# Optimization experiments

Hardware: AMD Instinct MI355X
Metric: run time of the kernel (lower is better)

The kernel has to match this reference:

```python
import jax, jax.numpy as jnp
import numpy as np

B, L, D, H = 2, 4096, 512, 8
HD = D // H  # head_dim = 64


def setup_inputs() -> dict:
    key = jax.random.key(0)
    ks = jax.random.split(key, 5)
    s = 0.02
    return {
        "x": jax.random.normal(ks[0], (B, L, D), dtype=jnp.float32),
        "w_qkv": jax.random.normal(ks[1], (D, 3 * D), dtype=jnp.float32) * s,
        "b_qkv": jax.random.normal(ks[2], (3 * D,), dtype=jnp.float32) * s,
        "w_o": jax.random.normal(ks[3], (D, D), dtype=jnp.float32) * s,
        "b_o": jax.random.normal(ks[4], (D,), dtype=jnp.float32) * s,
    }


def reference(x, w_qkv, b_qkv, w_o, b_o):
    b, l, _ = x.shape
    # QKV projection, then split heads: [B, L, 3D] -> [B, H, L, 3*HD]
    qkv = x @ w_qkv + b_qkv
    qkv = qkv.reshape(b, l, H, 3 * HD).transpose(0, 2, 1, 3)
    q, k, v = jnp.split(qkv, 3, axis=-1)  # each [B, H, L, HD]
    scale = 1.0 / jnp.sqrt(jnp.asarray(HD, dtype=q.dtype))
    # full score matrix [B, H, L, L], softmax in float32 (matches .float() cast)
    scores = jnp.einsum('bhld,bhsd->bhls', q, k) * scale
    attn = jax.nn.softmax(scores.astype(jnp.float32), axis=-1).astype(q.dtype)
    values = jnp.einsum('bhls,bhsd->bhld', attn, v)  # [B, H, L, HD]
    values = values.transpose(0, 2, 1, 3).reshape(b, l, D)
    return values @ w_o + b_o
```

## Files before the change

### kernel.cpp

```cpp
#include <hip/hip_runtime.h>


#define B_  2
#define L_  4096
#define D_  512
#define H_  8
#define HD_ 64
#define BH_ (B_*H_)
#define M_  (B_*L_)
#define QKVN (3*D_)
#define HEADSZ (BH_*L_*HD_)

typedef unsigned short ushort;
typedef unsigned int uint;
typedef __bf16 bf16x8 __attribute__((ext_vector_type(8)));
typedef float  f32x4  __attribute__((ext_vector_type(4)));
typedef float  f32x16 __attribute__((ext_vector_type(16)));

typedef const __attribute__((address_space(1))) void g_void;
typedef __attribute__((address_space(3))) void l_void;

#define C2_ 0.18033688011112042f

#if __has_builtin(__builtin_amdgcn_exp2f)
#define FEXP2(x) __builtin_amdgcn_exp2f(x)
#else
#define FEXP2(x) exp2f(x)
#endif

__device__ __forceinline__ ushort f2bf(float f) {
    __bf16 h = (__bf16)f;
    return __builtin_bit_cast(ushort, h);
}

__device__ __forceinline__ uint pack2(float lo, float hi) {
    return (uint)f2bf(lo) | ((uint)f2bf(hi) << 16);
}

__global__ __launch_bounds__(256)
void prep_k(const float* __restrict__ x, ushort* __restrict__ xb,
            const float* __restrict__ wq, ushort* __restrict__ wtq,
            const float* __restrict__ wo, ushort* __restrict__ wto)
{
    int bid = blockIdx.x, tid = threadIdx.x;
    if (bid < 4096) {
        int idx = bid * 256 + tid;
        float4 v = ((const float4*)x)[idx];
        ushort4 o; o.x = f2bf(v.x); o.y = f2bf(v.y); o.z = f2bf(v.z); o.w = f2bf(v.w);
        ((ushort4*)xb)[idx] = o;
    } else if (bid < 7168) {
        int idx = (bid - 4096) * 256 + tid;
        int c = idx / D_, r = idx % D_;
        wtq[idx] = f2bf(wq[r * QKVN + c]);
    } else {
        int idx = (bid - 7168) * 256 + tid;
        int c = idx / D_, r = idx % D_;
        wto[idx] = f2bf(wo[r * D_ + c]);
    }
}

template<int BN>
__global__ __launch_bounds__(256)
void gemm_bt(const ushort* __restrict__ A, const ushort* __restrict__ Bt,
             const float* __restrict__ bias, void* __restrict__ out,
             int M, int N, int K, int mode)
{
    constexpr int MT = (BN == 128) ? 4 : 2;
    constexpr int BL = BN / 64;
    __shared__ ushort As[2][128 * 32];
    __shared__ ushort Bs[2][BN * 32];

    const int tid  = threadIdx.x;
    const int lane = tid & 63;
    const int wid  = tid >> 6;
    const int wm   = (BN == 128) ? (wid >> 1) : wid;
    const int wn   = (BN == 128) ? (wid & 1) : 0;
    const int lr   = lane & 15;
    const int quad = lane >> 4;
    const int tm = blockIdx.x, tn = blockIdx.y;

    f32x4 acc[MT][4] = {};
    const int arow = tm * 128;
    const int brow = tn * BN;

    auto STAGE = [&](int t) {
        const int k0 = t * 32;
        ushort* as = &As[t & 1][0];
        ushort* bs = &Bs[t & 1][0];
        #pragma unroll
        for (int i = 0; i < 2; i++) {
            int c   = i * 256 + tid;
            int row = c >> 2;
            int kk  = (c & 3) * 8;
            __builtin_amdgcn_global_load_lds(
                (g_void*)&A[(size_t)(arow + row) * K + k0 + kk],
                (l_void*)&as[c * 8], 16, 0, 0);
        }
        #pragma unroll
        for (int i = 0; i < BL; i++) {
            int c   = i * 256 + tid;
            int row = c >> 2;
            int kk  = (c & 3) * 8;
            __builtin_amdgcn_global_load_lds(
                (g_void*)&Bt[(size_t)(brow + row) * K + k0 + kk],
                (l_void*)&bs[c * 8], 16, 0, 0);
        }
    };

    const int NK = K / 32;
    STAGE(0);
    for (int t = 0; t < NK; t++) {
        __syncthreads();
        if (t + 1 < NK) STAGE(t + 1);
        const ushort* as = &As[t & 1][0];
        const ushort* bs = &Bs[t & 1][0];

        bf16x8 af[MT], bfr[4];
        #pragma unroll
        for (int mt = 0; mt < MT; mt++)
            af[mt] = *(const bf16x8*)&as[(wm * (MT * 16) + mt * 16 + lr) * 32 + quad * 8];
        #pragma unroll
        for (int nt = 0; nt < 4; nt++)
            bfr[nt] = *(const bf16x8*)&bs[(wn * 64 + nt * 16 + lr) * 32 + quad * 8];
        #pragma unroll
        for (int mt = 0; mt < MT; mt++)
            #pragma unroll
            for (int nt = 0; nt < 4; nt++)
                acc[mt][nt] = __builtin_amdgcn_mfma_f32_16x16x32_bf16(
                    af[mt], bfr[nt], acc[mt][nt], 0, 0, 0);
    }

    if (mode == 0) {
        #pragma unroll
        for (int nt = 0; nt < 4; nt++) {
            int col = tn * BN + wn * 64 + nt * 16 + lr;
            float bv = bias[col];
            #pragma unroll
            for (int mt = 0; mt < MT; mt++) {
                #pragma unroll
                for (int r = 0; r < 4; r++) {
                    int row = tm * 128 + wm * (MT * 16) + mt * 16 + quad * 4 + r;
                    ((float*)out)[(size_t)row * N + col] = acc[mt][nt][r] + bv;
                }
            }
        }
    } else {
        const int g     = (tn * BN + wn * 64) >> 6;
        const int which = g % 3;
        const int h     = g / 3;
        ushort* qkv = (ushort*)out;
        if (which != 2) {
            const float qscale = (which == 0) ? C2_ : 1.0f;
            #pragma unroll
            for (int nt = 0; nt < 4; nt++) {
                int d = nt * 16 + lr;
                float bv = bias[g * 64 + d];
                #pragma unroll
                for (int mt = 0; mt < MT; mt++) {
                    #pragma unroll
                    for (int r = 0; r < 4; r++) {
                        int row = tm * 128 + wm * (MT * 16) + mt * 16 + quad * 4 + r;
                        int b = row >> 12;
                        int l = row & (L_ - 1);
                        float v = (acc[mt][nt][r] + bv) * qscale;
                        qkv[which * HEADSZ + (((b * H_ + h) * L_ + l) * HD_) + d]
                            = f2bf(v);
                    }
                }
            }
        } else {
            ushort* vt = qkv + 2 * HEADSZ;
            #pragma unroll
            for (int nt = 0; nt < 4; nt++) {
                int d = nt * 16 + lr;
                float bv = bias[g * 64 + d];
                #pragma unroll
                for (int mt = 0; mt < MT; mt++) {
                    int row0 = tm * 128 + wm * (MT * 16) + mt * 16 + quad * 4;
                    int b = row0 >> 12;
                    int l = row0 & (L_ - 1);
                    ushort4 pk;
                    pk.x = f2bf(acc[mt][nt][0] + bv);
                    pk.y = f2bf(acc[mt][nt][1] + bv);
                    pk.z = f2bf(acc[mt][nt][2] + bv);
                    pk.w = f2bf(acc[mt][nt][3] + bv);
                    *(ushort4*)&vt[((size_t)(b * H_ + h) * HD_ + d) * L_ + l] = pk;
                }
            }
        }
    }
}

__global__ __launch_bounds__(512, 4)
void attn_k(const ushort* __restrict__ Q, const ushort* __restrict__ K,
            const ushort* __restrict__ VT, ushort* __restrict__ O)
{
    __shared__ __align__(16) ushort SMEM[24576];
    ushort* Ksm = SMEM;
    ushort* Vsm = SMEM + 8192;

    const int tid  = threadIdx.x;
    const int lane = tid & 63;
    const int wid  = tid >> 6;
    const int qw   = wid & 3;
    const int kh   = wid >> 2;
    const int l31  = lane & 31;
    const int hi   = lane >> 5;

    const int wg  = blockIdx.x;
    const int xcd = wg & 7, sl = wg >> 3;
    const int bh  = (xcd << 1) | (sl >> 5);
    const int q0  = (sl & 31) * 128;
    const size_t base = (size_t)bh * (L_ * HD_);

    const int sr = tid >> 3;
    const int sc = ((tid & 7) ^ (sr & 7)) * 8;
    const ushort* Kg = K  + base + sr * HD_ + sc;
    const ushort* Vg = VT + base + (size_t)sr * L_ + sc;

    bf16x8 qf[4];
    {
        const ushort* qp = Q + base + (size_t)(q0 + qw * 32 + l31) * HD_ + hi * 8;
        #pragma unroll
        for (int ks = 0; ks < 4; ks++) qf[ks] = *(const bf16x8*)(qp + ks * 16);
    }

    const int swz = (l31 & 7) << 4;
    int cbe[4];
    #pragma unroll
    for (int ks = 0; ks < 4; ks++) cbe[ks] = ((ks * 32 + hi * 16) ^ swz) >> 1;
    const int krW  = (kh * 32 + l31) * 64;
    const int kr0v = l31 * 64, kr1v = (32 + l31) * 64;

    const f32x16 Z = {};
    bf16x8 onesB;
    #pragma unroll
    for (int i = 0; i < 8; i++) onesB[i] = (__bf16)1.0f;

    f32x16 o0 = {}, o1 = {}, l_acc = {};
    f32x16 sE, sO;

    auto STAGE = [&](int tt) {
        __builtin_amdgcn_global_load_lds(
            (g_void*)(Kg + (size_t)tt * 64 * HD_),
            (l_void*)(Ksm + (tt & 1) * 4096 + tid * 8), 16, 0, 0);
        __builtin_amdgcn_global_load_lds(
            (g_void*)(Vg + tt * 64),
            (l_void*)(Vsm + (tt & 3) * 4096 + tid * 8), 16, 0, 0);
    };

    auto QK = [&](int tt, f32x16& S) {
        const ushort* kb = Ksm + (tt & 1) * 4096;
        {
            bf16x8 k0 = *(const bf16x8*)&kb[krW + cbe[0]];
            S = __builtin_amdgcn_mfma_f32_32x32x16_bf16(k0, qf[0], Z, 0, 0, 0);
        }
        #pragma unroll
        for (int ks = 1; ks < 4; ks++) {
            bf16x8 k0 = *(const bf16x8*)&kb[krW + cbe[ks]];
            S = __builtin_amdgcn_mfma_f32_32x32x16_bf16(k0, qf[ks], S, 0, 0, 0);
        }
    };

    auto SMPV = [&](int tp, f32x16& S) {
        const ushort* vb = Vsm + (tp & 3) * 4096;
        #pragma unroll
        for (int i = 0; i < 16; i++) S[i] = FEXP2(S[i]);
        #pragma unroll
        for (int kk = 0; kk < 2; kk++) {
            const int ks = kh * 2 + kk;
            const int r0 = 8 * kk;
            uint a0 = pack2(S[r0 + 0], S[r0 + 1]);
            uint a1 = pack2(S[r0 + 2], S[r0 + 3]);
            uint b0 = pack2(S[r0 + 4], S[r0 + 5]);
            uint b1 = pack2(S[r0 + 6], S[r0 + 7]);
            asm("v_permlane32_swap_b32 %0, %1" : "+v"(a0), "+v"(b0));
            asm("v_permlane32_swap_b32 %0, %1" : "+v"(a1), "+v"(b1));
            uint4 w; w.x = a0; w.y = a1; w.z = b0; w.w = b1;
            bf16x8 pa = __builtin_bit_cast(bf16x8, w);
            bf16x8 v0 = *(const bf16x8*)&vb[kr0v + cbe[ks]];
            bf16x8 v1 = *(const bf16x8*)&vb[kr1v + cbe[ks]];
            o0 = __builtin_amdgcn_mfma_f32_32x32x16_bf16(pa, v0, o0, 0, 0, 0);
            o1 = __builtin_amdgcn_mfma_f32_32x32x16_bf16(pa, v1, o1, 0, 0, 0);
            l_acc = __builtin_amdgcn_mfma_f32_32x32x16_bf16(pa, onesB, l_acc, 0, 0, 0);
        }
    };

    STAGE(0);

    for (int t = 0; t < L_ / 64; t += 2) {
        __syncthreads();
        STAGE(t + 1);
        QK(t, sE);
        if (t > 0) SMPV(t - 1, sO);
        __syncthreads();
        if (t + 2 < L_ / 64) STAGE(t + 2);
        QK(t + 1, sO);
        SMPV(t, sE);
    }
    SMPV(L_ / 64 - 1, sO);

    __syncthreads();
    float* red = (float*)SMEM;
    if (kh == 1) {
        float* p = red + (qw * 64 + lane) * 48;
        #pragma unroll
        for (int r = 0; r < 16; r++) {
            p[r] = o0[r]; p[16 + r] = o1[r]; p[32 + r] = l_acc[r];
        }
    }
    __syncthreads();
    if (kh == 0) {
        const float* p = red + (qw * 64 + lane) * 48;
        #pragma unroll
        for (int r = 0; r < 16; r++) {
            o0[r] += p[r]; o1[r] += p[16 + r]; l_acc[r] += p[32 + r];
        }
        const int b = bh >> 3, h = bh & 7;
        #pragma unroll
        for (int r = 0; r < 16; r++) {
            const int qrl = (r & 3) + 8 * (r >> 2) + 4 * hi;
            const float inv = 1.0f / l_acc[r];
            const size_t row = (size_t)(b * L_ + q0 + qw * 32 + qrl) * D_ + h * HD_ + l31;
            O[row]      = f2bf(o0[r] * inv);
            O[row + 32] = f2bf(o1[r] * inv);
        }
    }
}

extern "C" void kernel_launch(void* const* d_in, const int* in_sizes, int n_in,
                              void* d_out, int out_size, void* d_ws, size_t ws_size,
                              hipStream_t stream)
{
    const float* x     = (const float*)d_in[0];
    const float* w_qkv = (const float*)d_in[1];
    const float* b_qkv = (const float*)d_in[2];
    const float* w_o   = (const float*)d_in[3];
    const float* b_o   = (const float*)d_in[4];

    char* ws = (char*)d_ws;
    size_t o = 0;
    ushort* xb   = (ushort*)(ws + o); o += (size_t)M_ * D_ * 2;
    ushort* qkv  = (ushort*)(ws + o); o += (size_t)3 * HEADSZ * 2;
    ushort* attn = (ushort*)(ws + o); o += (size_t)M_ * D_ * 2;
    ushort* wtq  = (ushort*)(ws + o); o += (size_t)QKVN * D_ * 2;
    ushort* wto  = (ushort*)(ws + o);

    hipLaunchKernelGGL(prep_k, dim3(8192), dim3(256), 0, stream,
                       x, xb, w_qkv, wtq, w_o, wto);
    hipLaunchKernelGGL((gemm_bt<128>), dim3(M_ / 128, QKVN / 128), dim3(256), 0, stream,
                       xb, wtq, b_qkv, (void*)qkv, M_, QKVN, D_, 1);
    hipLaunchKernelGGL(attn_k, dim3(512), dim3(512), 0, stream,
                       qkv, qkv + HEADSZ, qkv + 2 * HEADSZ, attn);
    hipLaunchKernelGGL((gemm_bt<64>), dim3(M_ / 128, D_ / 64), dim3(256), 0, stream,
                       attn, wto, b_o, d_out, M_, D_, D_, 0);
}
```

Measured before the change: 204.3 us.

## Fuse prep, QKV GEMM, attention and output GEMM into one persistent kernel

```diff
diff --git a/kernel.cpp b/kernel.cpp
--- a/kernel.cpp
+++ b/kernel.cpp
@@ -10,6 +10,7 @@
 #define M_  (B_*L_)
 #define QKVN (3*D_)
 #define HEADSZ (BH_*L_*HD_)
+#define NBLK 512
 
 typedef unsigned short ushort;
 typedef unsigned int uint;
@@ -37,148 +38,152 @@
     return (uint)f2bf(lo) | ((uint)f2bf(hi) << 16);
 }
 
-__global__ __launch_bounds__(256)
-void prep_k(const float* __restrict__ x, ushort* __restrict__ xb,
-            const float* __restrict__ wq, ushort* __restrict__ wtq,
-            const float* __restrict__ wo, ushort* __restrict__ wto)
+__device__ uint g_cnt[4] = {0, 0, 0, 0};
+__device__ uint g_gen[4] = {0, 0, 0, 0};
+
+__device__ __forceinline__ void gbar(int i) {
+    __syncthreads();
+    if (threadIdx.x == 0) {
+        uint gen = __hip_atomic_load(&g_gen[i], __ATOMIC_ACQUIRE,
+                                     __HIP_MEMORY_SCOPE_AGENT);
+        __threadfence();
+        uint old = __hip_atomic_fetch_add(&g_cnt[i], 1u, __ATOMIC_ACQ_REL,
+                                          __HIP_MEMORY_SCOPE_AGENT);
+        if (old == (uint)NBLK - 1u) {
+            __hip_atomic_store(&g_cnt[i], 0u, __ATOMIC_RELAXED,
+                               __HIP_MEMORY_SCOPE_AGENT);
+            __hip_atomic_store(&g_gen[i], gen + 1u, __ATOMIC_RELEASE,
+                               __HIP_MEMORY_SCOPE_AGENT);
+        } else {
+            for (long k = 0; k < 10000000L; ++k) {
+                if (__hip_atomic_load(&g_gen[i], __ATOMIC_ACQUIRE,
+                                      __HIP_MEMORY_SCOPE_AGENT) != gen) break;
+                __builtin_amdgcn_s_sleep(4);
+            }
+        }
+        __threadfence();
+    }
+    __syncthreads();
+}
+
+__global__ __launch_bounds__(512, 4)
+void fused_k(const float* __restrict__ x,  const float* __restrict__ wq,
+             const float* __restrict__ bq, const float* __restrict__ wo,
+             const float* __restrict__ bo, char* __restrict__ ws,
+             float* __restrict__ out)
 {
-    int bid = blockIdx.x, tid = threadIdx.x;
-    if (bid < 4096) {
-        int idx = bid * 256 + tid;
-        float4 v = ((const float4*)x)[idx];
-        ushort4 o; o.x = f2bf(v.x); o.y = f2bf(v.y); o.z = f2bf(v.z); o.w = f2bf(v.w);
-        ((ushort4*)xb)[idx] = o;
-    } else if (bid < 7168) {
-        int idx = (bid - 4096) * 256 + tid;
-        int c = idx / D_, r = idx % D_;
-        wtq[idx] = f2bf(wq[r * QKVN + c]);
-    } else {
-        int idx = (bid - 7168) * 256 + tid;
-        int c = idx / D_, r = idx % D_;
-        wto[idx] = f2bf(wo[r * D_ + c]);
-    }
-}
-
-template<int BN>
-__global__ __launch_bounds__(256)
-void gemm_bt(const ushort* __restrict__ A, const ushort* __restrict__ Bt,
-             const float* __restrict__ bias, void* __restrict__ out,
-             int M, int N, int K, int mode)
-{
-    constexpr int MT = (BN == 128) ? 4 : 2;
-    constexpr int BL = BN / 64;
-    __shared__ ushort As[2][128 * 32];
-    __shared__ ushort Bs[2][BN * 32];
+    __shared__ __align__(16) ushort SMEM[24576];
+
+    ushort* xb  = (ushort*)ws;
+    ushort* qkv = (ushort*)(ws + (size_t)M_ * D_ * 2);
+    ushort* aO  = qkv + (size_t)3 * HEADSZ;
+    ushort* wtq = aO + (size_t)M_ * D_;
+    ushort* wto = wtq + (size_t)QKVN * D_;
 
     const int tid  = threadIdx.x;
+    const int wg   = blockIdx.x;
     const int lane = tid & 63;
     const int wid  = tid >> 6;
-    const int wm   = (BN == 128) ? (wid >> 1) : wid;
-    const int wn   = (BN == 128) ? (wid & 1) : 0;
     const int lr   = lane & 15;
     const int quad = lane >> 4;
-    const int tm = blockIdx.x, tn = blockIdx.y;
-
-    f32x4 acc[MT][4] = {};
-    const int arow = tm * 128;
-    const int brow = tn * BN;
-
-    auto STAGE = [&](int t) {
-        const int k0 = t * 32;
-        ushort* as = &As[t & 1][0];
-        ushort* bs = &Bs[t & 1][0];
-        #pragma unroll
-        for (int i = 0; i < 2; i++) {
-            int c   = i * 256 + tid;
-            int row = c >> 2;
-            int kk  = (c & 3) * 8;
-            __builtin_amdgcn_global_load_lds(
-                (g_void*)&A[(size_t)(arow + row) * K + k0 + kk],
-                (l_void*)&as[c * 8], 16, 0, 0);
-        }
-        #pragma unroll
-        for (int i = 0; i < BL; i++) {
-            int c   = i * 256 + tid;
-            int row = c >> 2;
-            int kk  = (c & 3) * 8;
-            __builtin_amdgcn_global_load_lds(
-                (g_void*)&Bt[(size_t)(brow + row) * K + k0 + kk],
-                (l_void*)&bs[c * 8], 16, 0, 0);
-        }
-    };
-
-    const int NK = K / 32;
-    STAGE(0);
-    for (int t = 0; t < NK; t++) {
-        __syncthreads();
-        if (t + 1 < NK) STAGE(t + 1);
-        const ushort* as = &As[t & 1][0];
-        const ushort* bs = &Bs[t & 1][0];
-
-        bf16x8 af[MT], bfr[4];
-        #pragma unroll
-        for (int mt = 0; mt < MT; mt++)
-            af[mt] = *(const bf16x8*)&as[(wm * (MT * 16) + mt * 16 + lr) * 32 + quad * 8];
-        #pragma unroll
-        for (int nt = 0; nt < 4; nt++)
-            bfr[nt] = *(const bf16x8*)&bs[(wn * 64 + nt * 16 + lr) * 32 + quad * 8];
-        #pragma unroll
-        for (int mt = 0; mt < MT; mt++)
-            #pragma unroll
-            for (int nt = 0; nt < 4; nt++)
-                acc[mt][nt] = __builtin_amdgcn_mfma_f32_16x16x32_bf16(
-                    af[mt], bfr[nt], acc[mt][nt], 0, 0, 0);
+
+    {
+        const int gtid = wg * 512 + tid;
+        #pragma unroll
+        for (int i = 0; i < 4; i++) {
+            int idx = i * 262144 + gtid;
+            float4 v = ((const float4*)x)[idx];
+            ushort4 o4; o4.x = f2bf(v.x); o4.y = f2bf(v.y);
+            o4.z = f2bf(v.z); o4.w = f2bf(v.w);
+            ((ushort4*)xb)[idx] = o4;
+        }
+        #pragma unroll
+        for (int i = 0; i < 3; i++) {
+            int idx = i * 262144 + gtid;
+            int c = idx / D_, r = idx % D_;
+            wtq[idx] = f2bf(wq[r * QKVN + c]);
+        }
+        {
+            int c = gtid / D_, r = gtid % D_;
+            wto[gtid] = f2bf(wo[r * D_ + c]);
+        }
     }
-
-    if (mode == 0) {
-        #pragma unroll
-        for (int nt = 0; nt < 4; nt++) {
-            int col = tn * BN + wn * 64 + nt * 16 + lr;
-            float bv = bias[col];
-            #pragma unroll
-            for (int mt = 0; mt < MT; mt++) {
+    gbar(0);
+
+    {
+        ushort* As = SMEM;
+        ushort* Bs = SMEM + 16384;
+        const int wm = wid >> 1, wn = wid & 1;
+        const int tm = wg >> 4, tn = wg & 15;
+        const int arow = tm * 256, brow = tn * 96;
+        f32x4 acc[4][3] = {};
+
+        auto STAGE = [&](int t) {
+            const int k0 = t * 32;
+            ushort* as = As + (t & 1) * 8192;
+            ushort* bs = Bs + (t & 1) * 3072;
+            #pragma unroll
+            for (int i = 0; i < 2; i++) {
+                int c = i * 512 + tid, row = c >> 2, kk = (c & 3) * 8;
+                __builtin_amdgcn_global_load_lds(
+                    (g_void*)&xb[(size_t)(arow + row) * D_ + k0 + kk],
+                    (l_void*)&as[c * 8], 16, 0, 0);
+            }
+            if (tid < 384) {
+                int c = tid, row = c >> 2, kk = (c & 3) * 8;
+                __builtin_amdgcn_global_load_lds(
+                    (g_void*)&wtq[(size_t)(brow + row) * D_ + k0 + kk],
+                    (l_void*)&bs[c * 8], 16, 0, 0);
+            }
+        };
+
+        STAGE(0);
+        for (int t = 0; t < 16; t++) {
+            __syncthreads();
+            if (t + 1 < 16) STAGE(t + 1);
+            const ushort* as = As + (t & 1) * 8192;
+            const ushort* bs = Bs + (t & 1) * 3072;
+            bf16x8 af[4], bfr[3];
+            #pragma unroll
+            for (int mt = 0; mt < 4; mt++)
+                af[mt] = *(const bf16x8*)&as[(wm * 64 + mt * 16 + lr) * 32 + quad * 8];
+            #pragma unroll
+            for (int nt = 0; nt < 3; nt++)
+                bfr[nt] = *(const bf16x8*)&bs[(wn * 48 + nt * 16 + lr) * 32 + quad * 8];
+            #pragma unroll
+            for (int mt = 0; mt < 4; mt++)
                 #pragma unroll
-                for (int r = 0; r < 4; r++) {
-                    int row = tm * 128 + wm * (MT * 16) + mt * 16 + quad * 4 + r;
-                    ((float*)out)[(size_t)row * N + col] = acc[mt][nt][r] + bv;
-                }
-            }
-        }
-    } else {
-        const int g     = (tn * BN + wn * 64) >> 6;
-        const int which = g % 3;
-        const int h     = g / 3;
-        ushort* qkv = (ushort*)out;
-        if (which != 2) {
-            const float qscale = (which == 0) ? C2_ : 1.0f;
-            #pragma unroll
-            for (int nt = 0; nt < 4; nt++) {
-                int d = nt * 16 + lr;
-                float bv = bias[g * 64 + d];
+                for (int nt = 0; nt < 3; nt++)
+                    acc[mt][nt] = __builtin_amdgcn_mfma_f32_16x16x32_bf16(
+                        af[mt], bfr[nt], acc[mt][nt], 0, 0, 0);
+        }
+
+        #pragma unroll
+        for (int nt = 0; nt < 3; nt++) {
+            const int col0  = tn * 96 + wn * 48 + nt * 16;
+            const int g     = col0 >> 6;
+            const int which = g % 3;
+            const int h     = g / 3;
+            const int d     = (col0 & 63) + lr;
+            const float bv  = bq[col0 + lr];
+            if (which != 2) {
+                const float qs = (which == 0) ? C2_ : 1.0f;
                 #pragma unroll
-                for (int mt = 0; mt < MT; mt++) {
+                for (int mt = 0; mt < 4; mt++) {
                     #pragma unroll
                     for (int r = 0; r < 4; r++) {
-                        int row = tm * 128 + wm * (MT * 16) + mt * 16 + quad * 4 + r;
-                        int b = row >> 12;
-                        int l = row & (L_ - 1);
-                        float v = (acc[mt][nt][r] + bv) * qscale;
+                        int row = tm * 256 + wm * 64 + mt * 16 + quad * 4 + r;
+                        int b = row >> 12, l = row & (L_ - 1);
                         qkv[which * HEADSZ + (((b * H_ + h) * L_ + l) * HD_) + d]
-                            = f2bf(v);
+                            = f2bf((acc[mt][nt][r] + bv) * qs);
                     }
                 }
-            }
-        } else {
-            ushort* vt = qkv + 2 * HEADSZ;
-            #pragma unroll
-            for (int nt = 0; nt < 4; nt++) {
-                int d = nt * 16 + lr;
-                float bv = bias[g * 64 + d];
+            } else {
+                ushort* vt = qkv + 2 * HEADSZ;
                 #pragma unroll
-                for (int mt = 0; mt < MT; mt++) {
-                    int row0 = tm * 128 + wm * (MT * 16) + mt * 16 + quad * 4;
-                    int b = row0 >> 12;
-                    int l = row0 & (L_ - 1);
+                for (int mt = 0; mt < 4; mt++) {
+                    int row0 = tm * 256 + wm * 64 + mt * 16 + quad * 4;
+                    int b = row0 >> 12, l = row0 & (L_ - 1);
                     ushort4 pk;
                     pk.x = f2bf(acc[mt][nt][0] + bv);
                     pk.y = f2bf(acc[mt][nt][1] + bv);
@@ -189,141 +194,192 @@
             }
         }
     }
-}
-
-__global__ __launch_bounds__(512, 4)
-void attn_k(const ushort* __restrict__ Q, const ushort* __restrict__ K,
-            const ushort* __restrict__ VT, ushort* __restrict__ O)
-{
-    __shared__ __align__(16) ushort SMEM[24576];
-    ushort* Ksm = SMEM;
-    ushort* Vsm = SMEM + 8192;
-
-    const int tid  = threadIdx.x;
-    const int lane = tid & 63;
-    const int wid  = tid >> 6;
-    const int qw   = wid & 3;
-    const int kh   = wid >> 2;
-    const int l31  = lane & 31;
-    const int hi   = lane >> 5;
-
-    const int wg  = blockIdx.x;
-    const int xcd = wg & 7, sl = wg >> 3;
-    const int bh  = (xcd << 1) | (sl >> 5);
-    const int q0  = (sl & 31) * 128;
-    const size_t base = (size_t)bh * (L_ * HD_);
-
-    const int sr = tid >> 3;
-    const int sc = ((tid & 7) ^ (sr & 7)) * 8;
-    const ushort* Kg = K  + base + sr * HD_ + sc;
-    const ushort* Vg = VT + base + (size_t)sr * L_ + sc;
-
-    bf16x8 qf[4];
+    gbar(1);
+
     {
-        const ushort* qp = Q + base + (size_t)(q0 + qw * 32 + l31) * HD_ + hi * 8;
-        #pragma unroll
-        for (int ks = 0; ks < 4; ks++) qf[ks] = *(const bf16x8*)(qp + ks * 16);
+        ushort* Ksm = SMEM;
+        ushort* Vsm = SMEM + 8192;
+
+        const int qw  = wid & 3;
+        const int kh  = wid >> 2;
+        const int l31 = lane & 31;
+        const int hi  = lane >> 5;
+
+        const int xcd = wg & 7, sl = wg >> 3;
+        const int bh  = (xcd << 1) | (sl >> 5);
+        const int q0  = (sl & 31) * 128;
+        const size_t base = (size_t)bh * (L_ * HD_);
+
+        const int sr = tid >> 3;
+        const int sc = ((tid & 7) ^ (sr & 7)) * 8;
+        const ushort* Q  = qkv;
+        const ushort* K  = qkv + HEADSZ;
+        const ushort* VT = qkv + 2 * HEADSZ;
+        const ushort* Kg = K  + base + sr * HD_ + sc;
+        const ushort* Vg = VT + base + (size_t)sr * L_ + sc;
+
+        bf16x8 qf[4];
+        {
+            const ushort* qp = Q + base + (size_t)(q0 + qw * 32 + l31) * HD_ + hi * 8;
+            #pragma unroll
+            for (int ks = 0; ks < 4; ks++) qf[ks] = *(const bf16x8*)(qp + ks * 16);
+        }
+
+        const int swz = (l31 & 7) << 4;
+        int cbe[4];
+        #pragma unroll
+        for (int ks = 0; ks < 4; ks++) cbe[ks] = ((ks * 32 + hi * 16) ^ swz) >> 1;
+        const int krW  = (kh * 32 + l31) * 64;
+        const int kr0v = l31 * 64, kr1v = (32 + l31) * 64;
+
+        const f32x16 Z = {};
+        bf16x8 onesB;
+        #pragma unroll
+        for (int i = 0; i < 8; i++) onesB[i] = (__bf16)1.0f;
+
+        f32x16 o0 = {}, o1 = {}, l_acc = {};
+        f32x16 sE, sO;
+
+        auto STAGE = [&](int tt) {
+            __builtin_amdgcn_global_load_lds(
+                (g_void*)(Kg + (size_t)tt * 64 * HD_),
+                (l_void*)(Ksm + (tt & 1) * 4096 + tid * 8), 16, 0, 0);
+            __builtin_amdgcn_global_load_lds(
+                (g_void*)(Vg + tt * 64),
+                (l_void*)(Vsm + (tt & 3) * 4096 + tid * 8), 16, 0, 0);
+        };
+
+        auto QK = [&](int tt, f32x16& S) {
+            const ushort* kb = Ksm + (tt & 1) * 4096;
+            {
+                bf16x8 k0 = *(const bf16x8*)&kb[krW + cbe[0]];
+                S = __builtin_amdgcn_mfma_f32_32x32x16_bf16(k0, qf[0], Z, 0, 0, 0);
+            }
+            #pragma unroll
+            for (int ks = 1; ks < 4; ks++) {
+                bf16x8 k0 = *(const bf16x8*)&kb[krW + cbe[ks]];
+                S = __builtin_amdgcn_mfma_f32_32x32x16_bf16(k0, qf[ks], S, 0, 0, 0);
+            }
+        };
+
+        auto SMPV = [&](int tp, f32x16& S) {
+            const ushort* vb = Vsm + (tp & 3) * 4096;
+            #pragma unroll
+            for (int i = 0; i < 16; i++) S[i] = FEXP2(S[i]);
+            #pragma unroll
+            for (int kk = 0; kk < 2; kk++) {
+                const int ks = kh * 2 + kk;
+                const int r0 = 8 * kk;
+                uint a0 = pack2(S[r0 + 0], S[r0 + 1]);
+                uint a1 = pack2(S[r0 + 2], S[r0 + 3]);
+                uint b0 = pack2(S[r0 + 4], S[r0 + 5]);
+                uint b1 = pack2(S[r0 + 6], S[r0 + 7]);
+                asm("v_permlane32_swap_b32 %0, %1" : "+v"(a0), "+v"(b0));
+                asm("v_permlane32_swap_b32 %0, %1" : "+v"(a1), "+v"(b1));
+                uint4 w; w.x = a0; w.y = a1; w.z = b0; w.w = b1;
+                bf16x8 pa = __builtin_bit_cast(bf16x8, w);
+                bf16x8 v0 = *(const bf16x8*)&vb[kr0v + cbe[ks]];
+                bf16x8 v1 = *(const bf16x8*)&vb[kr1v + cbe[ks]];
+                o0 = __builtin_amdgcn_mfma_f32_32x32x16_bf16(pa, v0, o0, 0, 0, 0);
+                o1 = __builtin_amdgcn_mfma_f32_32x32x16_bf16(pa, v1, o1, 0, 0, 0);
+                l_acc = __builtin_amdgcn_mfma_f32_32x32x16_bf16(pa, onesB, l_acc, 0, 0, 0);
+            }
+        };
+
+        STAGE(0);
+        for (int t = 0; t < L_ / 64; t += 2) {
+            __syncthreads();
+            STAGE(t + 1);
+            QK(t, sE);
+            if (t > 0) SMPV(t - 1, sO);
+            __syncthreads();
+            if (t + 2 < L_ / 64) STAGE(t + 2);
+            QK(t + 1, sO);
+            SMPV(t, sE);
+        }
+        SMPV(L_ / 64 - 1, sO);
+
+        __syncthreads();
+        float* red = (float*)SMEM;
+        if (kh == 1) {
+            float* p = red + (qw * 64 + lane) * 48;
+            #pragma unroll
+            for (int r = 0; r < 16; r++) {
+                p[r] = o0[r]; p[16 + r] = o1[r]; p[32 + r] = l_acc[r];
+            }
+        }
+        __syncthreads();
+        if (kh == 0) {
+            const float* p = red + (qw * 64 + lane) * 48;
+            #pragma unroll
+            for (int r = 0; r < 16; r++) {
+                o0[r] += p[r]; o1[r] += p[16 + r]; l_acc[r] += p[32 + r];
+            }
+            const int b = bh >> 3, h = bh & 7;
+            #pragma unroll
+            for (int r = 0; r < 16; r++) {
+                const int qrl = (r & 3) + 8 * (r >> 2) + 4 * hi;
+                const float inv = 1.0f / l_acc[r];
+                const size_t row = (size_t)(b * L_ + q0 + qw * 32 + qrl) * D_ + h * HD_ + l31;
+                aO[row]      = f2bf(o0[r] * inv);
+                aO[row + 32] = f2bf(o1[r] * inv);
+            }
+        }
     }
-
-    const int swz = (l31 & 7) << 4;
-    int cbe[4];
-    #pragma unroll
-    for (int ks = 0; ks < 4; ks++) cbe[ks] = ((ks * 32 + hi * 16) ^ swz) >> 1;
-    const int krW  = (kh * 32 + l31) * 64;
-    const int kr0v = l31 * 64, kr1v = (32 + l31) * 64;
-
-    const f32x16 Z = {};
-    bf16x8 onesB;
-    #pragma unroll
-    for (int i = 0; i < 8; i++) onesB[i] = (__bf16)1.0f;
-
-    f32x16 o0 = {}, o1 = {}, l_acc = {};
-    f32x16 sE, sO;
-
-    auto STAGE = [&](int tt) {
-        __builtin_amdgcn_global_load_lds(
-            (g_void*)(Kg + (size_t)tt * 64 * HD_),
-            (l_void*)(Ksm + (tt & 1) * 4096 + tid * 8), 16, 0, 0);
-        __builtin_amdgcn_global_load_lds(
-            (g_void*)(Vg + tt * 64),
-            (l_void*)(Vsm + (tt & 3) * 4096 + tid * 8), 16, 0, 0);
-    };
-
-    auto QK = [&](int tt, f32x16& S) {
-        const ushort* kb = Ksm + (tt & 1) * 4096;
-        {
-            bf16x8 k0 = *(const bf16x8*)&kb[krW + cbe[0]];
-            S = __builtin_amdgcn_mfma_f32_32x32x16_bf16(k0, qf[0], Z, 0, 0, 0);
-        }
-        #pragma unroll
-        for (int ks = 1; ks < 4; ks++) {
-            bf16x8 k0 = *(const bf16x8*)&kb[krW + cbe[ks]];
-            S = __builtin_amdgcn_mfma_f32_32x32x16_bf16(k0, qf[ks], S, 0, 0, 0);
-        }
-    };
-
-    auto SMPV = [&](int tp, f32x16& S) {
-        const ushort* vb = Vsm + (tp & 3) * 4096;
-        #pragma unroll
-        for (int i = 0; i < 16; i++) S[i] = FEXP2(S[i]);
-        #pragma unroll
-        for (int kk = 0; kk < 2; kk++) {
-            const int ks = kh * 2 + kk;
-            const int r0 = 8 * kk;
-            uint a0 = pack2(S[r0 + 0], S[r0 + 1]);
-            uint a1 = pack2(S[r0 + 2], S[r0 + 3]);
-            uint b0 = pack2(S[r0 + 4], S[r0 + 5]);
-            uint b1 = pack2(S[r0 + 6], S[r0 + 7]);
-            asm("v_permlane32_swap_b32 %0, %1" : "+v"(a0), "+v"(b0));
-            asm("v_permlane32_swap_b32 %0, %1" : "+v"(a1), "+v"(b1));
-            uint4 w; w.x = a0; w.y = a1; w.z = b0; w.w = b1;
-            bf16x8 pa = __builtin_bit_cast(bf16x8, w);
-            bf16x8 v0 = *(const bf16x8*)&vb[kr0v + cbe[ks]];
-            bf16x8 v1 = *(const bf16x8*)&vb[kr1v + cbe[ks]];
-            o0 = __builtin_amdgcn_mfma_f32_32x32x16_bf16(pa, v0, o0, 0, 0, 0);
-            o1 = __builtin_amdgcn_mfma_f32_32x32x16_bf16(pa, v1, o1, 0, 0, 0);
-            l_acc = __builtin_amdgcn_mfma_f32_32x32x16_bf16(pa, onesB, l_acc, 0, 0, 0);
-        }
-    };
-
-    STAGE(0);
-
-    for (int t = 0; t < L_ / 64; t += 2) {
+    gbar(2);
+
+    {
+        ushort* As = SMEM;
+        ushort* Bs = SMEM + 8192;
+        const int tm = wg >> 3, tn = wg & 7;
+        const int arow = tm * 128, brow = tn * 64;
+        f32x4 acc[4] = {};
+
+        auto STAGE = [&](int t) {
+            const int k0 = t * 32;
+            ushort* as = As + (t & 1) * 4096;
+            ushort* bs = Bs + (t & 1) * 2048;
+            {
+                int c = tid, row = c >> 2, kk = (c & 3) * 8;
+                __builtin_amdgcn_global_load_lds(
+                    (g_void*)&aO[(size_t)(arow + row) * D_ + k0 + kk],
+                    (l_void*)&as[c * 8], 16, 0, 0);
+            }
+            if (tid < 256) {
+                int c = tid, row = c >> 2, kk = (c & 3) * 8;
+                __builtin_amdgcn_global_load_lds(
+                    (g_void*)&wto[(size_t)(brow + row) * D_ + k0 + kk],
+                    (l_void*)&bs[c * 8], 16, 0, 0);
+            }
+        };
+
         __syncthreads();
-        STAGE(t + 1);
-        QK(t, sE);
-        if (t > 0) SMPV(t - 1, sO);
-        __syncthreads();
-        if (t + 2 < L_ / 64) STAGE(t + 2);
-        QK(t + 1, sO);
-        SMPV(t, sE);
-    }
-    SMPV(L_ / 64 - 1, sO);
-
-    __syncthreads();
-    float* red = (float*)SMEM;
-    if (kh == 1) {
-        float* p = red + (qw * 64 + lane) * 48;
-        #pragma unroll
-        for (int r = 0; r < 16; r++) {
-            p[r] = o0[r]; p[16 + r] = o1[r]; p[32 + r] = l_acc[r];
-        }
-    }
-    __syncthreads();
-    if (kh == 0) {
-        const float* p = red + (qw * 64 + lane) * 48;
-        #pragma unroll
-        for (int r = 0; r < 16; r++) {
-            o0[r] += p[r]; o1[r] += p[16 + r]; l_acc[r] += p[32 + r];
-        }
-        const int b = bh >> 3, h = bh & 7;
-        #pragma unroll
-        for (int r = 0; r < 16; r++) {
-            const int qrl = (r & 3) + 8 * (r >> 2) + 4 * hi;
-            const float inv = 1.0f / l_acc[r];
-            const size_t row = (size_t)(b * L_ + q0 + qw * 32 + qrl) * D_ + h * HD_ + l31;
-            O[row]      = f2bf(o0[r] * inv);
-            O[row + 32] = f2bf(o1[r] * inv);
+        STAGE(0);
+        for (int t = 0; t < 16; t++) {
+            __syncthreads();
+            if (t + 1 < 16) STAGE(t + 1);
+            const ushort* as = As + (t & 1) * 4096;
+            const ushort* bs = Bs + (t & 1) * 2048;
+            bf16x8 af = *(const bf16x8*)&as[(wid * 16 + lr) * 32 + quad * 8];
+            bf16x8 bfr[4];
+            #pragma unroll
+            for (int nt = 0; nt < 4; nt++)
+                bfr[nt] = *(const bf16x8*)&bs[(nt * 16 + lr) * 32 + quad * 8];
+            #pragma unroll
+            for (int nt = 0; nt < 4; nt++)
+                acc[nt] = __builtin_amdgcn_mfma_f32_16x16x32_bf16(
+                    af, bfr[nt], acc[nt], 0, 0, 0);
+        }
+
+        #pragma unroll
+        for (int nt = 0; nt < 4; nt++) {
+            int col = tn * 64 + nt * 16 + lr;
+            float bv = bo[col];
+            #pragma unroll
+            for (int r = 0; r < 4; r++) {
+                int row = tm * 128 + wid * 16 + quad * 4 + r;
+                out[(size_t)row * D_ + col] = acc[nt][r] + bv;
+            }
         }
     }
 }
@@ -337,21 +393,9 @@
     const float* b_qkv = (const float*)d_in[2];
     const float* w_o   = (const float*)d_in[3];
     const float* b_o   = (const float*)d_in[4];
-
-    char* ws = (char*)d_ws;
-    size_t o = 0;
-    ushort* xb   = (ushort*)(ws + o); o += (size_t)M_ * D_ * 2;
-    ushort* qkv  = (ushort*)(ws + o); o += (size_t)3 * HEADSZ * 2;
-    ushort* attn = (ushort*)(ws + o); o += (size_t)M_ * D_ * 2;
-    ushort* wtq  = (ushort*)(ws + o); o += (size_t)QKVN * D_ * 2;
-    ushort* wto  = (ushort*)(ws + o);
-
-    hipLaunchKernelGGL(prep_k, dim3(8192), dim3(256), 0, stream,
-                       x, xb, w_qkv, wtq, w_o, wto);
-    hipLaunchKernelGGL((gemm_bt<128>), dim3(M_ / 128, QKVN / 128), dim3(256), 0, stream,
-                       xb, wtq, b_qkv, (void*)qkv, M_, QKVN, D_, 1);
-    hipLaunchKernelGGL(attn_k, dim3(512), dim3(512), 0, stream,
-                       qkv, qkv + HEADSZ, qkv + 2 * HEADSZ, attn);
-    hipLaunchKernelGGL((gemm_bt<64>), dim3(M_ / 128, D_ / 64), dim3(256), 0, stream,
-                       attn, wto, b_o, d_out, M_, D_, D_, 0);
+    char*  ws  = (char*)d_ws;
+    float* op  = (float*)d_out;
+
+    hipLaunchKernelGGL(fused_k, dim3(NBLK), dim3(512), 0, stream,
+                       x, w_qkv, b_qkv, w_o, b_o, ws, op);
 }
```

New measurement: 483.2 us. 136% more time.
